# Kernel optimization log

Measured on AMD Instinct MI355X. Metric: run time of the kernel, lower is better.

The kernel has to match this reference:

```python
import jax, jax.numpy as jnp
import numpy as np


def setup_inputs() -> dict:
    key = jax.random.key(0)
    k1, k2, k3 = jax.random.split(key, 3)
    B, S, M, N = 4, 4, 1024, 8192
    ret = jax.random.normal(k1, (B, S * M * 3), dtype=jnp.float32)
    coords = jax.random.normal(k2, (B, N, 3), dtype=jnp.float32)
    labels = jax.random.randint(k3, (B, N, 1), 0, S).astype(jnp.float32)
    gt = jnp.concatenate([coords, labels], axis=-1)  # (B, N, 4)
    return {"ret": ret, "gt": gt, "seg_num_all": S}


def reference(ret, gt, seg_num_all):
    # part == 'part_dense' branch: per-part Chamfer-L1, averaged over
    # present parts per sample, then averaged over batch.
    B, N, _ = gt.shape
    S = seg_num_all
    pred = ret.reshape(B, S, -1, 3)          # (B,S,M,3)
    gtp = gt[..., :3]                         # (B,N,3)
    lab = gt[..., 3].astype(jnp.int32)        # (B,N)
    # part membership mask: (B,S,N)
    mask = lab[:, None, :] == jnp.arange(S, dtype=jnp.int32)[None, :, None]
    # pairwise squared distances pred part points vs all gt points: (B,S,M,N)
    d2 = (jnp.sum(pred * pred, -1)[..., None]
          + jnp.sum(gtp * gtp, -1)[:, None, None, :]
          - 2.0 * jnp.einsum('bsmc,bnc->bsmn', pred, gtp))
    d = jnp.sqrt(jnp.maximum(d2, 1e-12))      # L1-Chamfer uses sqrt of sq-dist
    BIG = jnp.asarray(1e10, d.dtype)
    # pred -> gt(part): min over gt points of the same part, mean over M
    d1 = jnp.min(jnp.where(mask[:, :, None, :], d, BIG), axis=3).mean(axis=2)  # (B,S)
    # gt(part) -> pred(part): min over the part's M pred points, masked mean over n
    dmin = jnp.min(d, axis=2)                 # (B,S,N)
    cnt = mask.sum(axis=-1)                   # (B,S)
    d2m = jnp.sum(jnp.where(mask, dmin, 0.0), axis=-1) / jnp.maximum(cnt, 1)
    chamfer = 0.5 * (d1 + d2m)                # (B,S) ChamferDistanceL1 per part
    present = cnt > 0
    chamfer = jnp.where(present, chamfer, 0.0)
    per_sample = chamfer.sum(axis=-1) / jnp.maximum(present.sum(axis=-1), 1)
    return per_sample.mean()
```

## Files before the change

### kernel.cpp

```cpp
#include <hip/hip_runtime.h>
#include <math.h>

namespace {

constexpr int kB = 4;
constexpr int kS = 4;
constexpr int kM = 1024;
constexpr int kN = 8192;
constexpr int kBS = kB * kS;
constexpr float kBig2 = 1e20f;

constexpr int OFF_D1 = 0;
constexpr int OFF_DM = OFF_D1 + kBS * kM;
constexpr int MINS_WORDS = kBS * kM + kBS * kN;
constexpr int OFF_C4 = MINS_WORDS;
constexpr int OFF_P4 = OFF_C4 + 4 * kBS * kN;
constexpr int OFF_CUR = OFF_P4 + 4 * kBS * kM;

constexpr int INIT_BLOCKS = MINS_WORDS / 1024;
constexpr int P4_BLOCKS = kBS * kM / 256;
constexpr int SCAT_BLOCKS = kB * kN / 256;

constexpr int NSPL1 = 16;
constexpr int K1_TILE = 128;
constexpr int K1_BLOCKS = kBS * NSPL1;
constexpr int GSPL = 2;
constexpr int MSPL = 8;
constexpr int K2_BLOCKS = kBS * GSPL * MSPL;

__global__ __launch_bounds__(256) void kprep(const float* __restrict__ ret,
                                             unsigned int* __restrict__ ws,
                                             float* __restrict__ out) {
  const int blk = blockIdx.x, tid = threadIdx.x;
  if (blk < INIT_BLOCKS) {
    ((uint4*)ws)[blk * 256 + tid] = make_uint4(~0u, ~0u, ~0u, ~0u);
    return;
  }
  if (blk < INIT_BLOCKS + P4_BLOCKS) {
    const int gi = (blk - INIT_BLOCKS) * 256 + tid;
    const float x = ret[gi * 3], y = ret[gi * 3 + 1], z = ret[gi * 3 + 2];
    ((float4*)(ws + OFF_P4))[gi] = make_float4(x, y, z, fmaf(x, x, fmaf(y, y, z * z)));
    return;
  }
  if (tid < kBS) ((int*)ws)[OFF_CUR + tid] = tid * kN;
  if (tid == kBS) out[0] = 0.f;
}

__global__ __launch_bounds__(256) void kscatter(const float4* __restrict__ gt,
                                                unsigned int* __restrict__ ws) {
  const int tid = threadIdx.x;
  const int idx = blockIdx.x * 256 + tid;
  const int b = idx >> 13;
  const int wave = tid >> 6, lane = tid & 63;
  const float4 q = gt[idx];
  const int s = (int)q.w;
  __shared__ int wcnt[4][kS];
  __shared__ int bbase[kS];
  int rank = 0;
#pragma unroll
  for (int ss = 0; ss < kS; ++ss) {
    const unsigned long long m = __ballot(s == ss);
    if (lane == 0) wcnt[wave][ss] = (int)__popcll(m);
    if (s == ss) rank = (int)__popcll(m & ((1ull << lane) - 1ull));
  }
  __syncthreads();
  if (tid < kS) {
    const int tot = wcnt[0][tid] + wcnt[1][tid] + wcnt[2][tid] + wcnt[3][tid];
    bbase[tid] = atomicAdd((int*)ws + OFF_CUR + b * kS + tid, tot);
  }
  __syncthreads();
  int pos = bbase[s] + rank;
#pragma unroll
  for (int w = 0; w < 4; ++w)
    if (w < wave) pos += wcnt[w][s];
  const float gn = fmaf(q.x, q.x, fmaf(q.y, q.y, q.z * q.z));
  ((float4*)(ws + OFF_C4))[pos] = make_float4(q.x, q.y, q.z, gn);
}

__global__ __launch_bounds__(256) void kdist(unsigned int* __restrict__ ws) {
  const int tid = threadIdx.x;
  __shared__ float4 tile[K1_TILE];
  const int* cur = (const int*)ws + OFF_CUR;
  const float4* c4 = (const float4*)(ws + OFF_C4);
  const float4* p4 = (const float4*)(ws + OFF_P4);

  if (blockIdx.x < K1_BLOCKS) {
    const int t = blockIdx.x & (NSPL1 - 1);
    const int bs = blockIdx.x >> 4;
    const int cnt = cur[bs] - bs * kN;
    const float4 P0 = p4[bs * kM + tid];
    const float4 P1 = p4[bs * kM + tid + 256];
    const float4 P2 = p4[bs * kM + tid + 512];
    const float4 P3 = p4[bs * kM + tid + 768];
    const float ax0 = -2.f * P0.x, ay0 = -2.f * P0.y, az0 = -2.f * P0.z;
    const float ax1 = -2.f * P1.x, ay1 = -2.f * P1.y, az1 = -2.f * P1.z;
    const float ax2 = -2.f * P2.x, ay2 = -2.f * P2.y, az2 = -2.f * P2.z;
    const float ax3 = -2.f * P3.x, ay3 = -2.f * P3.y, az3 = -2.f * P3.z;
    float b0 = kBig2, b1 = kBig2, b2 = kBig2, b3 = kBig2;
    for (int start = t * K1_TILE; start < cnt; start += NSPL1 * K1_TILE) {
      __syncthreads();
      if (tid < K1_TILE) {
        const int j = start + tid;
        tile[tid] = (j < cnt) ? c4[bs * kN + j] : make_float4(0.f, 0.f, 0.f, kBig2);
      }
      __syncthreads();
#pragma unroll 8
      for (int j = 0; j < K1_TILE; ++j) {
        const float4 g = tile[j];
        b0 = fminf(b0, fmaf(ax0, g.x, fmaf(ay0, g.y, fmaf(az0, g.z, g.w))));
        b1 = fminf(b1, fmaf(ax1, g.x, fmaf(ay1, g.y, fmaf(az1, g.z, g.w))));
        b2 = fminf(b2, fmaf(ax2, g.x, fmaf(ay2, g.y, fmaf(az2, g.z, g.w))));
        b3 = fminf(b3, fmaf(ax3, g.x, fmaf(ay3, g.y, fmaf(az3, g.z, g.w))));
      }
    }
    atomicMin(&ws[OFF_D1 + bs * kM + tid],       __float_as_uint(fmaxf(b0 + P0.w, 0.f)));
    atomicMin(&ws[OFF_D1 + bs * kM + tid + 256], __float_as_uint(fmaxf(b1 + P1.w, 0.f)));
    atomicMin(&ws[OFF_D1 + bs * kM + tid + 512], __float_as_uint(fmaxf(b2 + P2.w, 0.f)));
    atomicMin(&ws[OFF_D1 + bs * kM + tid + 768], __float_as_uint(fmaxf(b3 + P3.w, 0.f)));
  } else {
    int r = blockIdx.x - K1_BLOCKS;
    const int ms = r & (MSPL - 1); r >>= 3;
    const int gs = r & (GSPL - 1); r >>= 1;
    const int bs = r;
    const int cnt = cur[bs] - bs * kN;
    if (tid < K1_TILE) tile[tid] = p4[bs * kM + ms * K1_TILE + tid];
    __syncthreads();
    for (int base = gs * 1024; base < cnt; base += GSPL * 1024) {
      const int l0 = base + tid, l1 = l0 + 256, l2 = l0 + 512, l3 = l0 + 768;
      const bool v0 = l0 < cnt, v1 = l1 < cnt, v2 = l2 < cnt, v3 = l3 < cnt;
      const float4 G0 = v0 ? c4[bs * kN + l0] : make_float4(0.f, 0.f, 0.f, 0.f);
      const float4 G1 = v1 ? c4[bs * kN + l1] : make_float4(0.f, 0.f, 0.f, 0.f);
      const float4 G2 = v2 ? c4[bs * kN + l2] : make_float4(0.f, 0.f, 0.f, 0.f);
      const float4 G3 = v3 ? c4[bs * kN + l3] : make_float4(0.f, 0.f, 0.f, 0.f);
      const float ax0 = -2.f * G0.x, ay0 = -2.f * G0.y, az0 = -2.f * G0.z;
      const float ax1 = -2.f * G1.x, ay1 = -2.f * G1.y, az1 = -2.f * G1.z;
      const float ax2 = -2.f * G2.x, ay2 = -2.f * G2.y, az2 = -2.f * G2.z;
      const float ax3 = -2.f * G3.x, ay3 = -2.f * G3.y, az3 = -2.f * G3.z;
      float b0 = kBig2, b1 = kBig2, b2 = kBig2, b3 = kBig2;
#pragma unroll 8
      for (int mm = 0; mm < K1_TILE; ++mm) {
        const float4 p = tile[mm];
        b0 = fminf(b0, fmaf(ax0, p.x, fmaf(ay0, p.y, fmaf(az0, p.z, p.w))));
        b1 = fminf(b1, fmaf(ax1, p.x, fmaf(ay1, p.y, fmaf(az1, p.z, p.w))));
        b2 = fminf(b2, fmaf(ax2, p.x, fmaf(ay2, p.y, fmaf(az2, p.z, p.w))));
        b3 = fminf(b3, fmaf(ax3, p.x, fmaf(ay3, p.y, fmaf(az3, p.z, p.w))));
      }
      if (v0) atomicMin(&ws[OFF_DM + bs * kN + l0], __float_as_uint(fmaxf(b0 + G0.w, 0.f)));
      if (v1) atomicMin(&ws[OFF_DM + bs * kN + l1], __float_as_uint(fmaxf(b1 + G1.w, 0.f)));
      if (v2) atomicMin(&ws[OFF_DM + bs * kN + l2], __float_as_uint(fmaxf(b2 + G2.w, 0.f)));
      if (v3) atomicMin(&ws[OFF_DM + bs * kN + l3], __float_as_uint(fmaxf(b3 + G3.w, 0.f)));
    }
  }
}

__global__ __launch_bounds__(256) void krf(const unsigned int* __restrict__ ws,
                                           float* __restrict__ out) {
  const int tid = threadIdx.x, lane = tid & 63, wid = tid >> 6;
  const int bs = blockIdx.x, b = bs >> 2;
  const int* cur = (const int*)ws + OFF_CUR;
  const int cnt = cur[bs] - bs * kN;
  float s1 = 0.f;
  for (int m = tid; m < kM; m += 256)
    s1 += sqrtf(fmaxf(__uint_as_float(ws[OFF_D1 + bs * kM + m]), 1e-12f));
  float s2 = 0.f;
  for (int i = tid; i < cnt; i += 256)
    s2 += sqrtf(fmaxf(__uint_as_float(ws[OFF_DM + bs * kN + i]), 1e-12f));
  for (int o = 32; o > 0; o >>= 1) {
    s1 += __shfl_down(s1, o);
    s2 += __shfl_down(s2, o);
  }
  __shared__ float r1[4], r2[4];
  if (lane == 0) { r1[wid] = s1; r2[wid] = s2; }
  __syncthreads();
  if (tid == 0) {
    const float a1 = r1[0] + r1[1] + r1[2] + r1[3];
    const float a2 = r2[0] + r2[1] + r2[2] + r2[3];
    int pres = 0;
    for (int s = 0; s < kS; ++s) pres += (cur[b * kS + s] - (b * kS + s) * kN) > 0 ? 1 : 0;
    const float cham = cnt > 0 ? 0.5f * (a1 / (float)kM + a2 / (float)max(cnt, 1)) : 0.f;
    atomicAdd(out, cham / (float)(kB * max(pres, 1)));
  }
}

}

extern "C" void kernel_launch(void* const* d_in, const int* in_sizes, int n_in,
                              void* d_out, int out_size, void* d_ws, size_t ws_size,
                              hipStream_t stream) {
  const float* ret = (const float*)d_in[0];
  const float4* gt = (const float4*)d_in[1];
  unsigned int* ws = (unsigned int*)d_ws;
  float* out = (float*)d_out;

  kprep<<<INIT_BLOCKS + P4_BLOCKS + 1, 256, 0, stream>>>(ret, ws, out);
  kscatter<<<SCAT_BLOCKS, 256, 0, stream>>>(gt, ws);
  kdist<<<K1_BLOCKS + K2_BLOCKS, 256, 0, stream>>>(ws);
  krf<<<kBS, 256, 0, stream>>>(ws, out);
}
```

Baseline: 33.49 us.

## Replace atomicMin reductions with per-split partial planes and a deterministic histogram scatter

The distance kernel now writes per-split partial minima into separate planes instead of calling atomicMin on shared buffers, and the final kernel min-reduces those planes before the sqrt and sum. This removes the min-buffer initialisation pass and the atomic contention. The label scatter now counts labels per chunk first and uses prefix offsets, so it is deterministic and no longer needs atomic cursors. In exchange the reduction kernel reads several times more data using only 16 blocks, and the scatter runs on just 32 blocks.

```diff
diff --git a/kernel.cpp b/kernel.cpp
--- a/kernel.cpp
+++ b/kernel.cpp
@@ -10,17 +10,6 @@
 constexpr int kBS = kB * kS;
 constexpr float kBig2 = 1e20f;
 
-constexpr int OFF_D1 = 0;
-constexpr int OFF_DM = OFF_D1 + kBS * kM;
-constexpr int MINS_WORDS = kBS * kM + kBS * kN;
-constexpr int OFF_C4 = MINS_WORDS;
-constexpr int OFF_P4 = OFF_C4 + 4 * kBS * kN;
-constexpr int OFF_CUR = OFF_P4 + 4 * kBS * kM;
-
-constexpr int INIT_BLOCKS = MINS_WORDS / 1024;
-constexpr int P4_BLOCKS = kBS * kM / 256;
-constexpr int SCAT_BLOCKS = kB * kN / 256;
-
 constexpr int NSPL1 = 16;
 constexpr int K1_TILE = 128;
 constexpr int K1_BLOCKS = kBS * NSPL1;
@@ -28,66 +17,105 @@
 constexpr int MSPL = 8;
 constexpr int K2_BLOCKS = kBS * GSPL * MSPL;
 
-__global__ __launch_bounds__(256) void kprep(const float* __restrict__ ret,
-                                             unsigned int* __restrict__ ws,
-                                             float* __restrict__ out) {
+constexpr int NCHUNK = 32;
+
+constexpr int OFF_PD1 = 0;
+constexpr int OFF_PDM = OFF_PD1 + NSPL1 * kBS * kM;
+constexpr int OFF_C4 = OFF_PDM + MSPL * kBS * kN;
+constexpr int OFF_P4 = OFF_C4 + 4 * kBS * kN;
+constexpr int OFF_HIST = OFF_P4 + 4 * kBS * kM;
+constexpr int OFF_CNT = OFF_HIST + NCHUNK * kS;
+
+constexpr int P4_BLOCKS = kBS * kM / 256;
+
+__global__ __launch_bounds__(256) void kprepA(const float* __restrict__ ret,
+                                              const float4* __restrict__ gt,
+                                              unsigned int* __restrict__ ws,
+                                              float* __restrict__ out) {
   const int blk = blockIdx.x, tid = threadIdx.x;
-  if (blk < INIT_BLOCKS) {
-    ((uint4*)ws)[blk * 256 + tid] = make_uint4(~0u, ~0u, ~0u, ~0u);
+  if (blk < NCHUNK) {
+    const int wave = tid >> 6, lane = tid & 63;
+    int c0 = 0, c1 = 0, c2 = 0, c3 = 0;
+#pragma unroll
+    for (int r = 0; r < 4; ++r) {
+      const int s = (int)gt[blk * 1024 + r * 256 + tid].w;
+      const unsigned long long m0 = __ballot(s == 0);
+      const unsigned long long m1 = __ballot(s == 1);
+      const unsigned long long m2 = __ballot(s == 2);
+      const unsigned long long m3 = __ballot(s == 3);
+      if (lane == 0) {
+        c0 += (int)__popcll(m0); c1 += (int)__popcll(m1);
+        c2 += (int)__popcll(m2); c3 += (int)__popcll(m3);
+      }
+    }
+    __shared__ int wc[4][kS];
+    if (lane == 0) { wc[wave][0] = c0; wc[wave][1] = c1; wc[wave][2] = c2; wc[wave][3] = c3; }
+    __syncthreads();
+    if (tid < kS)
+      ((int*)ws)[OFF_HIST + blk * kS + tid] = wc[0][tid] + wc[1][tid] + wc[2][tid] + wc[3][tid];
+    if (blk == 0 && tid == 64) out[0] = 0.f;
     return;
   }
-  if (blk < INIT_BLOCKS + P4_BLOCKS) {
-    const int gi = (blk - INIT_BLOCKS) * 256 + tid;
-    const float x = ret[gi * 3], y = ret[gi * 3 + 1], z = ret[gi * 3 + 2];
-    ((float4*)(ws + OFF_P4))[gi] = make_float4(x, y, z, fmaf(x, x, fmaf(y, y, z * z)));
-    return;
-  }
-  if (tid < kBS) ((int*)ws)[OFF_CUR + tid] = tid * kN;
-  if (tid == kBS) out[0] = 0.f;
+  const int gi = (blk - NCHUNK) * 256 + tid;
+  const float x = ret[gi * 3], y = ret[gi * 3 + 1], z = ret[gi * 3 + 2];
+  ((float4*)(ws + OFF_P4))[gi] = make_float4(x, y, z, fmaf(x, x, fmaf(y, y, z * z)));
 }
 
 __global__ __launch_bounds__(256) void kscatter(const float4* __restrict__ gt,
                                                 unsigned int* __restrict__ ws) {
-  const int tid = threadIdx.x;
-  const int idx = blockIdx.x * 256 + tid;
-  const int b = idx >> 13;
+  const int c = blockIdx.x, tid = threadIdx.x;
+  const int b = c >> 3, cloc = c & 7;
   const int wave = tid >> 6, lane = tid & 63;
-  const float4 q = gt[idx];
-  const int s = (int)q.w;
+  __shared__ int hist[8][kS];
+  __shared__ int cursor[kS];
   __shared__ int wcnt[4][kS];
-  __shared__ int bbase[kS];
-  int rank = 0;
-#pragma unroll
-  for (int ss = 0; ss < kS; ++ss) {
-    const unsigned long long m = __ballot(s == ss);
-    if (lane == 0) wcnt[wave][ss] = (int)__popcll(m);
-    if (s == ss) rank = (int)__popcll(m & ((1ull << lane) - 1ull));
-  }
+  if (tid < 32) hist[tid >> 2][tid & 3] = ((const int*)ws)[OFF_HIST + (b * 8) * kS + tid];
   __syncthreads();
   if (tid < kS) {
-    const int tot = wcnt[0][tid] + wcnt[1][tid] + wcnt[2][tid] + wcnt[3][tid];
-    bbase[tid] = atomicAdd((int*)ws + OFF_CUR + b * kS + tid, tot);
+    int base = 0;
+    for (int cc = 0; cc < cloc; ++cc) base += hist[cc][tid];
+    cursor[tid] = base;
+  }
+  float4* c4 = (float4*)(ws + OFF_C4);
+#pragma unroll
+  for (int r = 0; r < 4; ++r) {
+    __syncthreads();
+    const float4 q = gt[c * 1024 + r * 256 + tid];
+    const int s = (int)q.w;
+    int rank = 0;
+#pragma unroll
+    for (int ss = 0; ss < kS; ++ss) {
+      const unsigned long long m = __ballot(s == ss);
+      if (lane == 0) wcnt[wave][ss] = (int)__popcll(m);
+      if (s == ss) rank = (int)__popcll(m & ((1ull << lane) - 1ull));
+    }
+    __syncthreads();
+    int pos = cursor[s] + rank;
+#pragma unroll
+    for (int w = 0; w < 4; ++w)
+      if (w < wave) pos += wcnt[w][s];
+    const float gn = fmaf(q.x, q.x, fmaf(q.y, q.y, q.z * q.z));
+    c4[(b * kS + s) * kN + pos] = make_float4(q.x, q.y, q.z, gn);
+    __syncthreads();
+    if (tid < kS) cursor[tid] += wcnt[0][tid] + wcnt[1][tid] + wcnt[2][tid] + wcnt[3][tid];
   }
   __syncthreads();
-  int pos = bbase[s] + rank;
-#pragma unroll
-  for (int w = 0; w < 4; ++w)
-    if (w < wave) pos += wcnt[w][s];
-  const float gn = fmaf(q.x, q.x, fmaf(q.y, q.y, q.z * q.z));
-  ((float4*)(ws + OFF_C4))[pos] = make_float4(q.x, q.y, q.z, gn);
+  if (cloc == 7 && tid < kS) ((int*)ws)[OFF_CNT + b * kS + tid] = cursor[tid];
 }
 
 __global__ __launch_bounds__(256) void kdist(unsigned int* __restrict__ ws) {
   const int tid = threadIdx.x;
   __shared__ float4 tile[K1_TILE];
-  const int* cur = (const int*)ws + OFF_CUR;
+  const int* cnt_p = (const int*)ws + OFF_CNT;
   const float4* c4 = (const float4*)(ws + OFF_C4);
   const float4* p4 = (const float4*)(ws + OFF_P4);
+  float* pd1 = (float*)(ws + OFF_PD1);
+  float* pdm = (float*)(ws + OFF_PDM);
 
   if (blockIdx.x < K1_BLOCKS) {
     const int t = blockIdx.x & (NSPL1 - 1);
     const int bs = blockIdx.x >> 4;
-    const int cnt = cur[bs] - bs * kN;
+    const int cnt = cnt_p[bs];
     const float4 P0 = p4[bs * kM + tid];
     const float4 P1 = p4[bs * kM + tid + 256];
     const float4 P2 = p4[bs * kM + tid + 512];
@@ -113,18 +141,20 @@
         b3 = fminf(b3, fmaf(ax3, g.x, fmaf(ay3, g.y, fmaf(az3, g.z, g.w))));
       }
     }
-    atomicMin(&ws[OFF_D1 + bs * kM + tid],       __float_as_uint(fmaxf(b0 + P0.w, 0.f)));
-    atomicMin(&ws[OFF_D1 + bs * kM + tid + 256], __float_as_uint(fmaxf(b1 + P1.w, 0.f)));
-    atomicMin(&ws[OFF_D1 + bs * kM + tid + 512], __float_as_uint(fmaxf(b2 + P2.w, 0.f)));
-    atomicMin(&ws[OFF_D1 + bs * kM + tid + 768], __float_as_uint(fmaxf(b3 + P3.w, 0.f)));
+    float* row = pd1 + t * (kBS * kM) + bs * kM + tid;
+    row[0] = b0 + P0.w;
+    row[256] = b1 + P1.w;
+    row[512] = b2 + P2.w;
+    row[768] = b3 + P3.w;
   } else {
     int r = blockIdx.x - K1_BLOCKS;
     const int ms = r & (MSPL - 1); r >>= 3;
     const int gs = r & (GSPL - 1); r >>= 1;
     const int bs = r;
-    const int cnt = cur[bs] - bs * kN;
+    const int cnt = cnt_p[bs];
     if (tid < K1_TILE) tile[tid] = p4[bs * kM + ms * K1_TILE + tid];
     __syncthreads();
+    float* plane = pdm + ms * (kBS * kN) + bs * kN;
     for (int base = gs * 1024; base < cnt; base += GSPL * 1024) {
       const int l0 = base + tid, l1 = l0 + 256, l2 = l0 + 512, l3 = l0 + 768;
       const bool v0 = l0 < cnt, v1 = l1 < cnt, v2 = l2 < cnt, v3 = l3 < cnt;
@@ -145,10 +175,10 @@
         b2 = fminf(b2, fmaf(ax2, p.x, fmaf(ay2, p.y, fmaf(az2, p.z, p.w))));
         b3 = fminf(b3, fmaf(ax3, p.x, fmaf(ay3, p.y, fmaf(az3, p.z, p.w))));
       }
-      if (v0) atomicMin(&ws[OFF_DM + bs * kN + l0], __float_as_uint(fmaxf(b0 + G0.w, 0.f)));
-      if (v1) atomicMin(&ws[OFF_DM + bs * kN + l1], __float_as_uint(fmaxf(b1 + G1.w, 0.f)));
-      if (v2) atomicMin(&ws[OFF_DM + bs * kN + l2], __float_as_uint(fmaxf(b2 + G2.w, 0.f)));
-      if (v3) atomicMin(&ws[OFF_DM + bs * kN + l3], __float_as_uint(fmaxf(b3 + G3.w, 0.f)));
+      if (v0) plane[l0] = b0 + G0.w;
+      if (v1) plane[l1] = b1 + G1.w;
+      if (v2) plane[l2] = b2 + G2.w;
+      if (v3) plane[l3] = b3 + G3.w;
     }
   }
 }
@@ -157,14 +187,24 @@
                                            float* __restrict__ out) {
   const int tid = threadIdx.x, lane = tid & 63, wid = tid >> 6;
   const int bs = blockIdx.x, b = bs >> 2;
-  const int* cur = (const int*)ws + OFF_CUR;
-  const int cnt = cur[bs] - bs * kN;
+  const int* cnt_p = (const int*)ws + OFF_CNT;
+  const int cnt = cnt_p[bs];
+  const float* pd1 = (const float*)(ws + OFF_PD1) + bs * kM;
+  const float* pdm = (const float*)(ws + OFF_PDM) + bs * kN;
   float s1 = 0.f;
-  for (int m = tid; m < kM; m += 256)
-    s1 += sqrtf(fmaxf(__uint_as_float(ws[OFF_D1 + bs * kM + m]), 1e-12f));
+  for (int m = tid; m < kM; m += 256) {
+    float u = pd1[m];
+#pragma unroll
+    for (int t = 1; t < NSPL1; ++t) u = fminf(u, pd1[t * (kBS * kM) + m]);
+    s1 += sqrtf(fmaxf(u, 1e-12f));
+  }
   float s2 = 0.f;
-  for (int i = tid; i < cnt; i += 256)
-    s2 += sqrtf(fmaxf(__uint_as_float(ws[OFF_DM + bs * kN + i]), 1e-12f));
+  for (int i = tid; i < cnt; i += 256) {
+    float u = pdm[i];
+#pragma unroll
+    for (int t = 1; t < MSPL; ++t) u = fminf(u, pdm[t * (kBS * kN) + i]);
+    s2 += sqrtf(fmaxf(u, 1e-12f));
+  }
   for (int o = 32; o > 0; o >>= 1) {
     s1 += __shfl_down(s1, o);
     s2 += __shfl_down(s2, o);
@@ -176,7 +216,7 @@
     const float a1 = r1[0] + r1[1] + r1[2] + r1[3];
     const float a2 = r2[0] + r2[1] + r2[2] + r2[3];
     int pres = 0;
-    for (int s = 0; s < kS; ++s) pres += (cur[b * kS + s] - (b * kS + s) * kN) > 0 ? 1 : 0;
+    for (int s = 0; s < kS; ++s) pres += cnt_p[b * kS + s] > 0 ? 1 : 0;
     const float cham = cnt > 0 ? 0.5f * (a1 / (float)kM + a2 / (float)max(cnt, 1)) : 0.f;
     atomicAdd(out, cham / (float)(kB * max(pres, 1)));
   }
@@ -192,8 +232,8 @@
   unsigned int* ws = (unsigned int*)d_ws;
   float* out = (float*)d_out;
 
-  kprep<<<INIT_BLOCKS + P4_BLOCKS + 1, 256, 0, stream>>>(ret, ws, out);
-  kscatter<<<SCAT_BLOCKS, 256, 0, stream>>>(gt, ws);
+  kprepA<<<NCHUNK + P4_BLOCKS, 256, 0, stream>>>(ret, gt, ws, out);
+  kscatter<<<NCHUNK, 256, 0, stream>>>(gt, ws);
   kdist<<<K1_BLOCKS + K2_BLOCKS, 256, 0, stream>>>(ws);
   krf<<<kBS, 256, 0, stream>>>(ws, out);
 }
```

Result: slower. 39.24 us (+17.2%).

## Fuse prep, scatter, distance and reduce kernels into one persistent kernel

Applied to the files above, without the earlier changes.

Merges the four launches into a single kernel of 512 blocks. The stages are separated by software grid barriers built on agent-scope atomics and a sleep-spin wait. A small memset clears the per-part counters and barrier words, and the counters now hold a count from zero rather than an absolute offset. The aim is to remove the launch gaps and kernel-boundary drains between stages. The trade-off is that correctness depends on all blocks being co-resident (launch bounds 256,2), and the spin barriers add their own latency.

```diff
diff --git a/kernel.cpp b/kernel.cpp
--- a/kernel.cpp
+++ b/kernel.cpp
@@ -10,175 +10,194 @@
 constexpr int kBS = kB * kS;
 constexpr float kBig2 = 1e20f;
 
+constexpr int NSPL1 = 16;
+constexpr int K1_TILE = 128;
+constexpr int K1_BLOCKS = kBS * NSPL1;
+constexpr int GSPL = 2;
+constexpr int MSPL = 8;
+constexpr int K2_BLOCKS = kBS * GSPL * MSPL;
+constexpr int GRID = K1_BLOCKS + K2_BLOCKS;
+
 constexpr int OFF_D1 = 0;
 constexpr int OFF_DM = OFF_D1 + kBS * kM;
 constexpr int MINS_WORDS = kBS * kM + kBS * kN;
 constexpr int OFF_C4 = MINS_WORDS;
 constexpr int OFF_P4 = OFF_C4 + 4 * kBS * kN;
 constexpr int OFF_CUR = OFF_P4 + 4 * kBS * kM;
+constexpr int OFF_BAR = OFF_CUR + kBS;
+constexpr int ZERO_WORDS = kBS + 2;
 
 constexpr int INIT_BLOCKS = MINS_WORDS / 1024;
 constexpr int P4_BLOCKS = kBS * kM / 256;
+constexpr int SCAT_BASE = INIT_BLOCKS + P4_BLOCKS;
 constexpr int SCAT_BLOCKS = kB * kN / 256;
 
-constexpr int NSPL1 = 16;
-constexpr int K1_TILE = 128;
-constexpr int K1_BLOCKS = kBS * NSPL1;
-constexpr int GSPL = 2;
-constexpr int MSPL = 8;
-constexpr int K2_BLOCKS = kBS * GSPL * MSPL;
-
-__global__ __launch_bounds__(256) void kprep(const float* __restrict__ ret,
-                                             unsigned int* __restrict__ ws,
-                                             float* __restrict__ out) {
-  const int blk = blockIdx.x, tid = threadIdx.x;
-  if (blk < INIT_BLOCKS) {
-    ((uint4*)ws)[blk * 256 + tid] = make_uint4(~0u, ~0u, ~0u, ~0u);
-    return;
-  }
-  if (blk < INIT_BLOCKS + P4_BLOCKS) {
-    const int gi = (blk - INIT_BLOCKS) * 256 + tid;
+__device__ __forceinline__ void grid_barrier(unsigned int* c, bool wait) {
+  __syncthreads();
+  if (threadIdx.x == 0) {
+    __threadfence();
+    __hip_atomic_fetch_add(c, 1u, __ATOMIC_RELEASE, __HIP_MEMORY_SCOPE_AGENT);
+    if (wait) {
+      while (__hip_atomic_load(c, __ATOMIC_ACQUIRE, __HIP_MEMORY_SCOPE_AGENT) < (unsigned)GRID)
+        __builtin_amdgcn_s_sleep(4);
+    }
+  }
+  __syncthreads();
+}
+
+__global__ __launch_bounds__(256, 2) void kfused(const float* __restrict__ ret,
+                                                 const float4* __restrict__ gt,
+                                                 unsigned int* __restrict__ ws,
+                                                 float* __restrict__ out) {
+  const int bid = blockIdx.x, tid = threadIdx.x;
+  __shared__ float4 tile[K1_TILE];
+  __shared__ int wcnt[4][kS];
+  __shared__ int bbase[kS];
+  __shared__ float r1[4], r2[4];
+
+  if (bid < INIT_BLOCKS) {
+    ((uint4*)ws)[bid * 256 + tid] = make_uint4(~0u, ~0u, ~0u, ~0u);
+  } else if (bid < SCAT_BASE) {
+    const int gi = (bid - INIT_BLOCKS) * 256 + tid;
     const float x = ret[gi * 3], y = ret[gi * 3 + 1], z = ret[gi * 3 + 2];
     ((float4*)(ws + OFF_P4))[gi] = make_float4(x, y, z, fmaf(x, x, fmaf(y, y, z * z)));
-    return;
-  }
-  if (tid < kBS) ((int*)ws)[OFF_CUR + tid] = tid * kN;
-  if (tid == kBS) out[0] = 0.f;
-}
-
-__global__ __launch_bounds__(256) void kscatter(const float4* __restrict__ gt,
-                                                unsigned int* __restrict__ ws) {
-  const int tid = threadIdx.x;
-  const int idx = blockIdx.x * 256 + tid;
-  const int b = idx >> 13;
-  const int wave = tid >> 6, lane = tid & 63;
-  const float4 q = gt[idx];
-  const int s = (int)q.w;
-  __shared__ int wcnt[4][kS];
-  __shared__ int bbase[kS];
-  int rank = 0;
+  } else if (bid < SCAT_BASE + SCAT_BLOCKS) {
+    const int idx = (bid - SCAT_BASE) * 256 + tid;
+    const int b = idx >> 13;
+    const int wave = tid >> 6, lane = tid & 63;
+    const float4 q = gt[idx];
+    const int s = (int)q.w;
+    int rank = 0;
 #pragma unroll
-  for (int ss = 0; ss < kS; ++ss) {
-    const unsigned long long m = __ballot(s == ss);
-    if (lane == 0) wcnt[wave][ss] = (int)__popcll(m);
-    if (s == ss) rank = (int)__popcll(m & ((1ull << lane) - 1ull));
-  }
-  __syncthreads();
-  if (tid < kS) {
-    const int tot = wcnt[0][tid] + wcnt[1][tid] + wcnt[2][tid] + wcnt[3][tid];
-    bbase[tid] = atomicAdd((int*)ws + OFF_CUR + b * kS + tid, tot);
-  }
-  __syncthreads();
-  int pos = bbase[s] + rank;
+    for (int ss = 0; ss < kS; ++ss) {
+      const unsigned long long m = __ballot(s == ss);
+      if (lane == 0) wcnt[wave][ss] = (int)__popcll(m);
+      if (s == ss) rank = (int)__popcll(m & ((1ull << lane) - 1ull));
+    }
+    __syncthreads();
+    if (tid < kS) {
+      const int tot = wcnt[0][tid] + wcnt[1][tid] + wcnt[2][tid] + wcnt[3][tid];
+      bbase[tid] = atomicAdd((int*)ws + OFF_CUR + b * kS + tid, tot);
+    }
+    __syncthreads();
+    int pos = bbase[s] + rank;
 #pragma unroll
-  for (int w = 0; w < 4; ++w)
-    if (w < wave) pos += wcnt[w][s];
-  const float gn = fmaf(q.x, q.x, fmaf(q.y, q.y, q.z * q.z));
-  ((float4*)(ws + OFF_C4))[pos] = make_float4(q.x, q.y, q.z, gn);
-}
-
-__global__ __launch_bounds__(256) void kdist(unsigned int* __restrict__ ws) {
-  const int tid = threadIdx.x;
-  __shared__ float4 tile[K1_TILE];
-  const int* cur = (const int*)ws + OFF_CUR;
-  const float4* c4 = (const float4*)(ws + OFF_C4);
-  const float4* p4 = (const float4*)(ws + OFF_P4);
-
-  if (blockIdx.x < K1_BLOCKS) {
-    const int t = blockIdx.x & (NSPL1 - 1);
-    const int bs = blockIdx.x >> 4;
-    const int cnt = cur[bs] - bs * kN;
-    const float4 P0 = p4[bs * kM + tid];
-    const float4 P1 = p4[bs * kM + tid + 256];
-    const float4 P2 = p4[bs * kM + tid + 512];
-    const float4 P3 = p4[bs * kM + tid + 768];
-    const float ax0 = -2.f * P0.x, ay0 = -2.f * P0.y, az0 = -2.f * P0.z;
-    const float ax1 = -2.f * P1.x, ay1 = -2.f * P1.y, az1 = -2.f * P1.z;
-    const float ax2 = -2.f * P2.x, ay2 = -2.f * P2.y, az2 = -2.f * P2.z;
-    const float ax3 = -2.f * P3.x, ay3 = -2.f * P3.y, az3 = -2.f * P3.z;
-    float b0 = kBig2, b1 = kBig2, b2 = kBig2, b3 = kBig2;
-    for (int start = t * K1_TILE; start < cnt; start += NSPL1 * K1_TILE) {
+    for (int w = 0; w < 4; ++w)
+      if (w < wave) pos += wcnt[w][s];
+    const float gn = fmaf(q.x, q.x, fmaf(q.y, q.y, q.z * q.z));
+    ((float4*)(ws + OFF_C4))[(b * kS + s) * kN + pos] = make_float4(q.x, q.y, q.z, gn);
+  } else if (bid == GRID - 1 && tid == 0) {
+    out[0] = 0.f;
+  }
+
+  grid_barrier(&ws[OFF_BAR], true);
+
+  {
+    const float4* c4 = (const float4*)(ws + OFF_C4);
+    const float4* p4 = (const float4*)(ws + OFF_P4);
+    if (bid < K1_BLOCKS) {
+      const int t = bid & (NSPL1 - 1);
+      const int bs = bid >> 4;
+      const int cnt = (int)__hip_atomic_load(&ws[OFF_CUR + bs], __ATOMIC_RELAXED,
+                                             __HIP_MEMORY_SCOPE_AGENT);
+      const float4 P0 = p4[bs * kM + tid];
+      const float4 P1 = p4[bs * kM + tid + 256];
+      const float4 P2 = p4[bs * kM + tid + 512];
+      const float4 P3 = p4[bs * kM + tid + 768];
+      const float ax0 = -2.f * P0.x, ay0 = -2.f * P0.y, az0 = -2.f * P0.z;
+      const float ax1 = -2.f * P1.x, ay1 = -2.f * P1.y, az1 = -2.f * P1.z;
+      const float ax2 = -2.f * P2.x, ay2 = -2.f * P2.y, az2 = -2.f * P2.z;
+      const float ax3 = -2.f * P3.x, ay3 = -2.f * P3.y, az3 = -2.f * P3.z;
+      float b0 = kBig2, b1 = kBig2, b2 = kBig2, b3 = kBig2;
+      for (int start = t * K1_TILE; start < cnt; start += NSPL1 * K1_TILE) {
+        __syncthreads();
+        if (tid < K1_TILE) {
+          const int j = start + tid;
+          tile[tid] = (j < cnt) ? c4[bs * kN + j] : make_float4(0.f, 0.f, 0.f, kBig2);
+        }
+        __syncthreads();
+#pragma unroll 8
+        for (int j = 0; j < K1_TILE; ++j) {
+          const float4 g = tile[j];
+          b0 = fminf(b0, fmaf(ax0, g.x, fmaf(ay0, g.y, fmaf(az0, g.z, g.w))));
+          b1 = fminf(b1, fmaf(ax1, g.x, fmaf(ay1, g.y, fmaf(az1, g.z, g.w))));
+          b2 = fminf(b2, fmaf(ax2, g.x, fmaf(ay2, g.y, fmaf(az2, g.z, g.w))));
+          b3 = fminf(b3, fmaf(ax3, g.x, fmaf(ay3, g.y, fmaf(az3, g.z, g.w))));
+        }
+      }
+      atomicMin(&ws[OFF_D1 + bs * kM + tid],       __float_as_uint(fmaxf(b0 + P0.w, 0.f)));
+      atomicMin(&ws[OFF_D1 + bs * kM + tid + 256], __float_as_uint(fmaxf(b1 + P1.w, 0.f)));
+      atomicMin(&ws[OFF_D1 + bs * kM + tid + 512], __float_as_uint(fmaxf(b2 + P2.w, 0.f)));
+      atomicMin(&ws[OFF_D1 + bs * kM + tid + 768], __float_as_uint(fmaxf(b3 + P3.w, 0.f)));
+    } else {
+      int r = bid - K1_BLOCKS;
+      const int ms = r & (MSPL - 1); r >>= 3;
+      const int gs = r & (GSPL - 1); r >>= 1;
+      const int bs = r;
+      const int cnt = (int)__hip_atomic_load(&ws[OFF_CUR + bs], __ATOMIC_RELAXED,
+                                             __HIP_MEMORY_SCOPE_AGENT);
+      if (tid < K1_TILE) tile[tid] = p4[bs * kM + ms * K1_TILE + tid];
       __syncthreads();
-      if (tid < K1_TILE) {
-        const int j = start + tid;
-        tile[tid] = (j < cnt) ? c4[bs * kN + j] : make_float4(0.f, 0.f, 0.f, kBig2);
+      for (int base = gs * 1024; base < cnt; base += GSPL * 1024) {
+        const int l0 = base + tid, l1 = l0 + 256, l2 = l0 + 512, l3 = l0 + 768;
+        const bool v0 = l0 < cnt, v1 = l1 < cnt, v2 = l2 < cnt, v3 = l3 < cnt;
+        const float4 G0 = v0 ? c4[bs * kN + l0] : make_float4(0.f, 0.f, 0.f, 0.f);
+        const float4 G1 = v1 ? c4[bs * kN + l1] : make_float4(0.f, 0.f, 0.f, 0.f);
+        const float4 G2 = v2 ? c4[bs * kN + l2] : make_float4(0.f, 0.f, 0.f, 0.f);
+        const float4 G3 = v3 ? c4[bs * kN + l3] : make_float4(0.f, 0.f, 0.f, 0.f);
+        const float ax0 = -2.f * G0.x, ay0 = -2.f * G0.y, az0 = -2.f * G0.z;
+        const float ax1 = -2.f * G1.x, ay1 = -2.f * G1.y, az1 = -2.f * G1.z;
+        const float ax2 = -2.f * G2.x, ay2 = -2.f * G2.y, az2 = -2.f * G2.z;
+        const float ax3 = -2.f * G3.x, ay3 = -2.f * G3.y, az3 = -2.f * G3.z;
+        float b0 = kBig2, b1 = kBig2, b2 = kBig2, b3 = kBig2;
+#pragma unroll 8
+        for (int mm = 0; mm < K1_TILE; ++mm) {
+          const float4 p = tile[mm];
+          b0 = fminf(b0, fmaf(ax0, p.x, fmaf(ay0, p.y, fmaf(az0, p.z, p.w))));
+          b1 = fminf(b1, fmaf(ax1, p.x, fmaf(ay1, p.y, fmaf(az1, p.z, p.w))));
+          b2 = fminf(b2, fmaf(ax2, p.x, fmaf(ay2, p.y, fmaf(az2, p.z, p.w))));
+          b3 = fminf(b3, fmaf(ax3, p.x, fmaf(ay3, p.y, fmaf(az3, p.z, p.w))));
+        }
+        if (v0) atomicMin(&ws[OFF_DM + bs * kN + l0], __float_as_uint(fmaxf(b0 + G0.w, 0.f)));
+        if (v1) atomicMin(&ws[OFF_DM + bs * kN + l1], __float_as_uint(fmaxf(b1 + G1.w, 0.f)));
+        if (v2) atomicMin(&ws[OFF_DM + bs * kN + l2], __float_as_uint(fmaxf(b2 + G2.w, 0.f)));
+        if (v3) atomicMin(&ws[OFF_DM + bs * kN + l3], __float_as_uint(fmaxf(b3 + G3.w, 0.f)));
       }
-      __syncthreads();
-#pragma unroll 8
-      for (int j = 0; j < K1_TILE; ++j) {
-        const float4 g = tile[j];
-        b0 = fminf(b0, fmaf(ax0, g.x, fmaf(ay0, g.y, fmaf(az0, g.z, g.w))));
-        b1 = fminf(b1, fmaf(ax1, g.x, fmaf(ay1, g.y, fmaf(az1, g.z, g.w))));
-        b2 = fminf(b2, fmaf(ax2, g.x, fmaf(ay2, g.y, fmaf(az2, g.z, g.w))));
-        b3 = fminf(b3, fmaf(ax3, g.x, fmaf(ay3, g.y, fmaf(az3, g.z, g.w))));
+    }
+  }
+
+  grid_barrier(&ws[OFF_BAR + 1], bid < kBS);
+  if (bid >= kBS) return;
+
+  {
+    const int bs = bid, b = bs >> 2;
+    const int lane = tid & 63, wid = tid >> 6;
+    const int cnt = (int)__hip_atomic_load(&ws[OFF_CUR + bs], __ATOMIC_RELAXED,
+                                           __HIP_MEMORY_SCOPE_AGENT);
+    float s1 = 0.f;
+    for (int m = tid; m < kM; m += 256)
+      s1 += sqrtf(fmaxf(__uint_as_float(ws[OFF_D1 + bs * kM + m]), 1e-12f));
+    float s2 = 0.f;
+    for (int i = tid; i < cnt; i += 256)
+      s2 += sqrtf(fmaxf(__uint_as_float(ws[OFF_DM + bs * kN + i]), 1e-12f));
+    for (int o = 32; o > 0; o >>= 1) {
+      s1 += __shfl_down(s1, o);
+      s2 += __shfl_down(s2, o);
+    }
+    if (lane == 0) { r1[wid] = s1; r2[wid] = s2; }
+    __syncthreads();
+    if (tid == 0) {
+      const float a1 = r1[0] + r1[1] + r1[2] + r1[3];
+      const float a2 = r2[0] + r2[1] + r2[2] + r2[3];
+      int pres = 0;
+      for (int s = 0; s < kS; ++s) {
+        const int cs = (int)__hip_atomic_load(&ws[OFF_CUR + b * kS + s], __ATOMIC_RELAXED,
+                                              __HIP_MEMORY_SCOPE_AGENT);
+        pres += cs > 0 ? 1 : 0;
       }
-    }
-    atomicMin(&ws[OFF_D1 + bs * kM + tid],       __float_as_uint(fmaxf(b0 + P0.w, 0.f)));
-    atomicMin(&ws[OFF_D1 + bs * kM + tid + 256], __float_as_uint(fmaxf(b1 + P1.w, 0.f)));
-    atomicMin(&ws[OFF_D1 + bs * kM + tid + 512], __float_as_uint(fmaxf(b2 + P2.w, 0.f)));
-    atomicMin(&ws[OFF_D1 + bs * kM + tid + 768], __float_as_uint(fmaxf(b3 + P3.w, 0.f)));
-  } else {
-    int r = blockIdx.x - K1_BLOCKS;
-    const int ms = r & (MSPL - 1); r >>= 3;
-    const int gs = r & (GSPL - 1); r >>= 1;
-    const int bs = r;
-    const int cnt = cur[bs] - bs * kN;
-    if (tid < K1_TILE) tile[tid] = p4[bs * kM + ms * K1_TILE + tid];
-    __syncthreads();
-    for (int base = gs * 1024; base < cnt; base += GSPL * 1024) {
-      const int l0 = base + tid, l1 = l0 + 256, l2 = l0 + 512, l3 = l0 + 768;
-      const bool v0 = l0 < cnt, v1 = l1 < cnt, v2 = l2 < cnt, v3 = l3 < cnt;
-      const float4 G0 = v0 ? c4[bs * kN + l0] : make_float4(0.f, 0.f, 0.f, 0.f);
-      const float4 G1 = v1 ? c4[bs * kN + l1] : make_float4(0.f, 0.f, 0.f, 0.f);
-      const float4 G2 = v2 ? c4[bs * kN + l2] : make_float4(0.f, 0.f, 0.f, 0.f);
-      const float4 G3 = v3 ? c4[bs * kN + l3] : make_float4(0.f, 0.f, 0.f, 0.f);
-      const float ax0 = -2.f * G0.x, ay0 = -2.f * G0.y, az0 = -2.f * G0.z;
-      const float ax1 = -2.f * G1.x, ay1 = -2.f * G1.y, az1 = -2.f * G1.z;
-      const float ax2 = -2.f * G2.x, ay2 = -2.f * G2.y, az2 = -2.f * G2.z;
-      const float ax3 = -2.f * G3.x, ay3 = -2.f * G3.y, az3 = -2.f * G3.z;
-      float b0 = kBig2, b1 = kBig2, b2 = kBig2, b3 = kBig2;
-#pragma unroll 8
-      for (int mm = 0; mm < K1_TILE; ++mm) {
-        const float4 p = tile[mm];
-        b0 = fminf(b0, fmaf(ax0, p.x, fmaf(ay0, p.y, fmaf(az0, p.z, p.w))));
-        b1 = fminf(b1, fmaf(ax1, p.x, fmaf(ay1, p.y, fmaf(az1, p.z, p.w))));
-        b2 = fminf(b2, fmaf(ax2, p.x, fmaf(ay2, p.y, fmaf(az2, p.z, p.w))));
-        b3 = fminf(b3, fmaf(ax3, p.x, fmaf(ay3, p.y, fmaf(az3, p.z, p.w))));
-      }
-      if (v0) atomicMin(&ws[OFF_DM + bs * kN + l0], __float_as_uint(fmaxf(b0 + G0.w, 0.f)));
-      if (v1) atomicMin(&ws[OFF_DM + bs * kN + l1], __float_as_uint(fmaxf(b1 + G1.w, 0.f)));
-      if (v2) atomicMin(&ws[OFF_DM + bs * kN + l2], __float_as_uint(fmaxf(b2 + G2.w, 0.f)));
-      if (v3) atomicMin(&ws[OFF_DM + bs * kN + l3], __float_as_uint(fmaxf(b3 + G3.w, 0.f)));
-    }
-  }
-}
-
-__global__ __launch_bounds__(256) void krf(const unsigned int* __restrict__ ws,
-                                           float* __restrict__ out) {
-  const int tid = threadIdx.x, lane = tid & 63, wid = tid >> 6;
-  const int bs = blockIdx.x, b = bs >> 2;
-  const int* cur = (const int*)ws + OFF_CUR;
-  const int cnt = cur[bs] - bs * kN;
-  float s1 = 0.f;
-  for (int m = tid; m < kM; m += 256)
-    s1 += sqrtf(fmaxf(__uint_as_float(ws[OFF_D1 + bs * kM + m]), 1e-12f));
-  float s2 = 0.f;
-  for (int i = tid; i < cnt; i += 256)
-    s2 += sqrtf(fmaxf(__uint_as_float(ws[OFF_DM + bs * kN + i]), 1e-12f));
-  for (int o = 32; o > 0; o >>= 1) {
-    s1 += __shfl_down(s1, o);
-    s2 += __shfl_down(s2, o);
-  }
-  __shared__ float r1[4], r2[4];
-  if (lane == 0) { r1[wid] = s1; r2[wid] = s2; }
-  __syncthreads();
-  if (tid == 0) {
-    const float a1 = r1[0] + r1[1] + r1[2] + r1[3];
-    const float a2 = r2[0] + r2[1] + r2[2] + r2[3];
-    int pres = 0;
-    for (int s = 0; s < kS; ++s) pres += (cur[b * kS + s] - (b * kS + s) * kN) > 0 ? 1 : 0;
-    const float cham = cnt > 0 ? 0.5f * (a1 / (float)kM + a2 / (float)max(cnt, 1)) : 0.f;
-    atomicAdd(out, cham / (float)(kB * max(pres, 1)));
+      const float cham = cnt > 0 ? 0.5f * (a1 / (float)kM + a2 / (float)max(cnt, 1)) : 0.f;
+      atomicAdd(out, cham / (float)(kB * max(pres, 1)));
+    }
   }
 }
 
@@ -190,10 +209,7 @@
   const float* ret = (const float*)d_in[0];
   const float4* gt = (const float4*)d_in[1];
   unsigned int* ws = (unsigned int*)d_ws;
-  float* out = (float*)d_out;
-
-  kprep<<<INIT_BLOCKS + P4_BLOCKS + 1, 256, 0, stream>>>(ret, ws, out);
-  kscatter<<<SCAT_BLOCKS, 256, 0, stream>>>(gt, ws);
-  kdist<<<K1_BLOCKS + K2_BLOCKS, 256, 0, stream>>>(ws);
-  krf<<<kBS, 256, 0, stream>>>(ws, out);
-}
+
+  hipMemsetAsync((char*)d_ws + (size_t)OFF_CUR * 4, 0, ZERO_WORDS * 4, stream);
+  kfused<<<GRID, 256, 0, stream>>>(ret, gt, ws, (float*)d_out);
+}
```

Measured after the change: 90.44 us. 2.7x slower.
